# Kernel tuning notes

Measured on AMD Instinct MI355X. Metric: run time of the kernel, lower is better.

Reference implementation:

```python
import jax, jax.numpy as jnp
import numpy as np

B, N, D, F, E, K = 4, 2048, 1024, 4096, 16, 2
EPS = 1e-5  # torch LayerNorm default


def setup_inputs() -> dict:
    key = jax.random.key(0)
    ks = jax.random.split(key, 6)
    scaled = lambda k, shape, fan: jax.random.normal(k, shape, jnp.float32) / np.float32(np.sqrt(fan))
    return {
        "x": jax.random.normal(ks[0], (B, N, D), jnp.float32),
        "Wr": scaled(ks[1], (D, E), D),
        "br": jnp.zeros((E,), jnp.float32),
        "W1": scaled(ks[2], (E, D, F), D),
        "W3": scaled(ks[3], (E, D, F), D),
        "W2": scaled(ks[4], (E, F, D), F),
        "gamma": jnp.ones((E, D), jnp.float32),
        "beta": jnp.zeros((E, D), jnp.float32),
    }


def reference(x, Wr, br, W1, W3, W2, gamma, beta):
    b, n, d = x.shape
    e = Wr.shape[1]
    xf = x.reshape(-1, d)  # [T, D]

    # Router: softmax -> top-2 -> renormalize (eval mode: no noise)
    logits = xf @ Wr + br                      # [T, E]
    probs = jax.nn.softmax(logits, axis=-1)
    vals, idx = jax.lax.top_k(probs, K)        # [T, K]
    w = vals / vals.sum(axis=-1, keepdims=True)

    # Per-token per-expert combine weights [T, E] (0 for unselected experts)
    combine = jnp.zeros((xf.shape[0], e), x.dtype)
    for k in range(K):
        combine = combine + w[:, k:k + 1] * jax.nn.one_hot(idx[:, k], e, dtype=x.dtype)

    # Expert FFN (SwiGLU -> LayerNorm), weighted combine.
    # Computing each expert on all tokens and scaling by combine (0 where not
    # routed) is mathematically identical to the masked gather/scatter loop,
    # since SwiGLU+LayerNorm are per-token ops.
    out = jnp.zeros_like(xf)
    for ei in range(e):
        h = jax.nn.silu(xf @ W1[ei]) * (xf @ W3[ei])   # [T, F]
        y = h @ W2[ei]                                  # [T, D]
        mu = y.mean(axis=-1, keepdims=True)
        var = ((y - mu) ** 2).mean(axis=-1, keepdims=True)
        y = (y - mu) * jax.lax.rsqrt(var + EPS) * gamma[ei] + beta[ei]
        out = out + combine[:, ei:ei + 1] * y
    return out.reshape(b, n, d)
```

## Files before the change

### kernel.cpp

```cpp
#include <hip/hip_runtime.h>
#include <stdint.h>

#define T_TOK 8192
#define DD 1024
#define FF 4096
#define EE 16
#define BM 128
#define BN 128
#define BK 32
#define MAX_MT 144
#define MAX_SLOTS 18432

typedef __attribute__((ext_vector_type(4))) float f32x4;
typedef __attribute__((ext_vector_type(8))) short bf16x8;

__device__ __forceinline__ unsigned short f2bf(float f) {
  union { float f; unsigned u; } v; v.f = f;
  unsigned r = v.u + 0x7FFFu + ((v.u >> 16) & 1u);
  return (unsigned short)(r >> 16);
}

__device__ __forceinline__ void gload16(const void* g, void* l) {
  __builtin_amdgcn_global_load_lds(
      (const __attribute__((address_space(1))) unsigned int*)g,
      (__attribute__((address_space(3))) unsigned int*)l, 16, 0, 0);
}

__global__ void router_kernel(const float* __restrict__ x, const float* __restrict__ Wr,
                              const float* __restrict__ br,
                              int* __restrict__ counts, int* __restrict__ tok_e,
                              int* __restrict__ tok_s, float* __restrict__ tok_w,
                              int* __restrict__ elist) {
  int t = blockIdx.x * blockDim.x + threadIdx.x;
  if (t >= T_TOK) return;
  float acc[EE];
#pragma unroll
  for (int e = 0; e < EE; ++e) acc[e] = br[e];
  const f32x4* x4 = (const f32x4*)(x + (size_t)t * DD);
  for (int d4 = 0; d4 < DD / 4; ++d4) {
    f32x4 xv = x4[d4];
    const float* wr = Wr + (size_t)d4 * 4 * EE;
#pragma unroll
    for (int dd = 0; dd < 4; ++dd)
#pragma unroll
      for (int e = 0; e < EE; ++e) acc[e] += xv[dd] * wr[dd * EE + e];
  }
  int i0 = 0; float v0 = acc[0];
#pragma unroll
  for (int e = 1; e < EE; ++e) if (acc[e] > v0) { v0 = acc[e]; i0 = e; }
  int i1 = -1; float v1 = -3.4e38f;
#pragma unroll
  for (int e = 0; e < EE; ++e) if (e != i0 && acc[e] > v1) { v1 = acc[e]; i1 = e; }
  float p1 = __expf(v1 - v0);
  float w0 = 1.f / (1.f + p1);
  float w1 = p1 * w0;
  int s0 = atomicAdd(&counts[i0], 1);
  int s1 = atomicAdd(&counts[i1], 1);
  tok_e[2 * t] = i0; tok_s[2 * t] = s0; tok_w[2 * t] = w0;
  tok_e[2 * t + 1] = i1; tok_s[2 * t + 1] = s1; tok_w[2 * t + 1] = w1;
  elist[(size_t)i0 * T_TOK + s0] = t;
  elist[(size_t)i1 * T_TOK + s1] = t;
}

__global__ void scan_kernel(const int* __restrict__ counts, int* __restrict__ off,
                            int* __restrict__ mtb) {
  if (threadIdx.x == 0 && blockIdx.x == 0) {
    int o = 0, m = 0;
    for (int e = 0; e < EE; ++e) {
      off[e] = o; mtb[e] = m;
      int c = counts[e];
      int mt = (c + BM - 1) / BM;
      o += mt * BM; m += mt;
    }
    off[EE] = o; mtb[EE] = m;
  }
}

__global__ void gather_kernel(const float* __restrict__ x, const int* __restrict__ counts,
                              const int* __restrict__ off, const int* __restrict__ elist,
                              unsigned short* __restrict__ Xg) {
  int slot = blockIdx.x;
  if (slot >= off[EE]) return;
  int e = 0;
  while (e < EE - 1 && off[e + 1] <= slot) ++e;
  int s = slot - off[e];
  int tid = threadIdx.x;
  ushort4* dst = (ushort4*)(Xg + (size_t)slot * DD);
  if (s < counts[e]) {
    int t = elist[(size_t)e * T_TOK + s];
    f32x4 v = ((const f32x4*)(x + (size_t)t * DD))[tid];
    ushort4 o;
    o.x = f2bf(v[0]); o.y = f2bf(v[1]); o.z = f2bf(v[2]); o.w = f2bf(v[3]);
    dst[tid] = o;
  } else {
    ushort4 z; z.x = z.y = z.z = z.w = 0;
    dst[tid] = z;
  }
}

__global__ void transpose_conv(const float* __restrict__ src0, unsigned short* __restrict__ dst0,
                               int R, int C) {
  __shared__ float tile[64][65];
  int e = blockIdx.z;
  const float* src = src0 + (size_t)e * R * C;
  unsigned short* dst = dst0 + (size_t)e * R * C;
  int r0 = blockIdx.y * 64, c0 = blockIdx.x * 64;
  int tx = threadIdx.x & 15, ty = threadIdx.x >> 4;
#pragma unroll
  for (int i = 0; i < 4; ++i) {
    int r = i * 16 + ty;
    f32x4 v = *(const f32x4*)(src + (size_t)(r0 + r) * C + c0 + tx * 4);
    tile[r][tx * 4 + 0] = v[0]; tile[r][tx * 4 + 1] = v[1];
    tile[r][tx * 4 + 2] = v[2]; tile[r][tx * 4 + 3] = v[3];
  }
  __syncthreads();
#pragma unroll
  for (int i = 0; i < 4; ++i) {
    int c = i * 16 + ty;
    ushort4 o;
    o.x = f2bf(tile[tx * 4 + 0][c]); o.y = f2bf(tile[tx * 4 + 1][c]);
    o.z = f2bf(tile[tx * 4 + 2][c]); o.w = f2bf(tile[tx * 4 + 3][c]);
    *(ushort4*)(dst + (size_t)(c0 + c) * R + r0 + tx * 4) = o;
  }
}

__global__ __launch_bounds__(256, 2) void gemm1_kernel(
    const unsigned short* __restrict__ Xg, const unsigned short* __restrict__ W1t,
    const unsigned short* __restrict__ W3t, const int* __restrict__ off,
    const int* __restrict__ mtb, unsigned short* __restrict__ H) {
  __shared__ __align__(16) unsigned short As[BM][BK];
  __shared__ __align__(16) unsigned short B1s[BN][BK];
  __shared__ __align__(16) unsigned short B3s[BN][BK];
  int ty = blockIdx.y;
  if (ty >= mtb[EE]) return;
  int e = 0;
  while (e < EE - 1 && mtb[e + 1] <= ty) ++e;
  int m0 = off[e] + (ty - mtb[e]) * BM;
  int n0 = blockIdx.x * BN;
  const unsigned short* A = Xg + (size_t)m0 * DD;
  const unsigned short* B1 = W1t + ((size_t)e * FF + n0) * DD;
  const unsigned short* B3 = W3t + ((size_t)e * FF + n0) * DD;
  int tid = threadIdx.x, lane = tid & 63, wid = tid >> 6;
  int wm = wid >> 1, wn = wid & 1;
  f32x4 acc1[4][4] = {}; f32x4 acc3[4][4] = {};
  int fr = lane & 15, fk = (lane >> 4) * 8;
  for (int k0 = 0; k0 < DD; k0 += BK) {
#pragma unroll
    for (int r = 0; r < 2; ++r) {
      int c = r * 256 + tid;
      int row = c >> 2, ch = c & 3;
      gload16(A + (size_t)row * DD + k0 + ch * 8, (char*)As + c * 16);
      gload16(B1 + (size_t)row * DD + k0 + ch * 8, (char*)B1s + c * 16);
      gload16(B3 + (size_t)row * DD + k0 + ch * 8, (char*)B3s + c * 16);
    }
    __syncthreads();
    bf16x8 a[4], b1[4], b3[4];
#pragma unroll
    for (int mi = 0; mi < 4; ++mi) a[mi] = *(const bf16x8*)&As[wm * 64 + mi * 16 + fr][fk];
#pragma unroll
    for (int ni = 0; ni < 4; ++ni) {
      b1[ni] = *(const bf16x8*)&B1s[wn * 64 + ni * 16 + fr][fk];
      b3[ni] = *(const bf16x8*)&B3s[wn * 64 + ni * 16 + fr][fk];
    }
#pragma unroll
    for (int mi = 0; mi < 4; ++mi)
#pragma unroll
      for (int ni = 0; ni < 4; ++ni) {
        acc1[mi][ni] = __builtin_amdgcn_mfma_f32_16x16x32_bf16(a[mi], b1[ni], acc1[mi][ni], 0, 0, 0);
        acc3[mi][ni] = __builtin_amdgcn_mfma_f32_16x16x32_bf16(a[mi], b3[ni], acc3[mi][ni], 0, 0, 0);
      }
    __syncthreads();
  }
#pragma unroll
  for (int mi = 0; mi < 4; ++mi)
#pragma unroll
    for (int ni = 0; ni < 4; ++ni)
#pragma unroll
      for (int i = 0; i < 4; ++i) {
        int row = m0 + wm * 64 + mi * 16 + (lane >> 4) * 4 + i;
        int col = n0 + wn * 64 + ni * 16 + (lane & 15);
        float c1 = acc1[mi][ni][i], c3 = acc3[mi][ni][i];
        float h = c1 / (1.f + __expf(-c1)) * c3;
        H[(size_t)row * FF + col] = f2bf(h);
      }
}

__global__ __launch_bounds__(256, 2) void gemm2_kernel(
    const unsigned short* __restrict__ H, const unsigned short* __restrict__ W2t,
    const int* __restrict__ off, const int* __restrict__ mtb, float* __restrict__ Y) {
  __shared__ __align__(16) unsigned short As[BM][BK];
  __shared__ __align__(16) unsigned short Bs[BN][BK];
  int ty = blockIdx.y;
  if (ty >= mtb[EE]) return;
  int e = 0;
  while (e < EE - 1 && mtb[e + 1] <= ty) ++e;
  int m0 = off[e] + (ty - mtb[e]) * BM;
  int n0 = blockIdx.x * BN;
  const unsigned short* A = H + (size_t)m0 * FF;
  const unsigned short* B = W2t + ((size_t)e * DD + n0) * FF;
  int tid = threadIdx.x, lane = tid & 63, wid = tid >> 6;
  int wm = wid >> 1, wn = wid & 1;
  f32x4 acc[4][4] = {};
  int fr = lane & 15, fk = (lane >> 4) * 8;
  for (int k0 = 0; k0 < FF; k0 += BK) {
#pragma unroll
    for (int r = 0; r < 2; ++r) {
      int c = r * 256 + tid;
      int row = c >> 2, ch = c & 3;
      gload16(A + (size_t)row * FF + k0 + ch * 8, (char*)As + c * 16);
      gload16(B + (size_t)row * FF + k0 + ch * 8, (char*)Bs + c * 16);
    }
    __syncthreads();
    bf16x8 a[4], b[4];
#pragma unroll
    for (int mi = 0; mi < 4; ++mi) a[mi] = *(const bf16x8*)&As[wm * 64 + mi * 16 + fr][fk];
#pragma unroll
    for (int ni = 0; ni < 4; ++ni) b[ni] = *(const bf16x8*)&Bs[wn * 64 + ni * 16 + fr][fk];
#pragma unroll
    for (int mi = 0; mi < 4; ++mi)
#pragma unroll
      for (int ni = 0; ni < 4; ++ni)
        acc[mi][ni] = __builtin_amdgcn_mfma_f32_16x16x32_bf16(a[mi], b[ni], acc[mi][ni], 0, 0, 0);
    __syncthreads();
  }
#pragma unroll
  for (int mi = 0; mi < 4; ++mi)
#pragma unroll
    for (int ni = 0; ni < 4; ++ni)
#pragma unroll
      for (int i = 0; i < 4; ++i) {
        int row = m0 + wm * 64 + mi * 16 + (lane >> 4) * 4 + i;
        int col = n0 + wn * 64 + ni * 16 + (lane & 15);
        Y[(size_t)row * DD + col] = acc[mi][ni][i];
      }
}

__global__ void ln_combine_kernel(const float* __restrict__ Y, const int* __restrict__ tok_e,
                                  const int* __restrict__ tok_s, const float* __restrict__ tok_w,
                                  const int* __restrict__ off, const float* __restrict__ gamma,
                                  const float* __restrict__ beta, float* __restrict__ out) {
  int t = blockIdx.x, tid = threadIdx.x;
  __shared__ float red[8];
  f32x4 o = {0.f, 0.f, 0.f, 0.f};
  for (int k = 0; k < 2; ++k) {
    int e = tok_e[2 * t + k], s = tok_s[2 * t + k];
    float w = tok_w[2 * t + k];
    int slot = off[e] + s;
    f32x4 v = ((const f32x4*)(Y + (size_t)slot * DD))[tid];
    float sum = v[0] + v[1] + v[2] + v[3];
    float sq = v[0] * v[0] + v[1] * v[1] + v[2] * v[2] + v[3] * v[3];
    for (int d = 32; d > 0; d >>= 1) {
      sum += __shfl_down(sum, d);
      sq += __shfl_down(sq, d);
    }
    int wv = tid >> 6, lane = tid & 63;
    if (lane == 0) { red[wv * 2] = sum; red[wv * 2 + 1] = sq; }
    __syncthreads();
    float S1 = red[0] + red[2] + red[4] + red[6];
    float S2 = red[1] + red[3] + red[5] + red[7];
    __syncthreads();
    float mu = S1 * (1.f / (float)DD);
    float var = S2 * (1.f / (float)DD) - mu * mu;
    float rs = rsqrtf(var + 1e-5f);
    f32x4 g = ((const f32x4*)(gamma + (size_t)e * DD))[tid];
    f32x4 b = ((const f32x4*)(beta + (size_t)e * DD))[tid];
#pragma unroll
    for (int j = 0; j < 4; ++j) o[j] += w * ((v[j] - mu) * rs * g[j] + b[j]);
  }
  ((f32x4*)out)[(size_t)t * (DD / 4) + tid] = o;
}

extern "C" void kernel_launch(void* const* d_in, const int* in_sizes, int n_in,
                              void* d_out, int out_size, void* d_ws, size_t ws_size,
                              hipStream_t stream) {
  const float* x = (const float*)d_in[0];
  const float* Wr = (const float*)d_in[1];
  const float* br = (const float*)d_in[2];
  const float* W1 = (const float*)d_in[3];
  const float* W3 = (const float*)d_in[4];
  const float* W2 = (const float*)d_in[5];
  const float* gamma = (const float*)d_in[6];
  const float* beta = (const float*)d_in[7];
  float* out = (float*)d_out;

  char* w = (char*)d_ws;
  size_t o = 0;
  auto alloc = [&](size_t bytes) {
    void* p = w + o;
    o += (bytes + 255) & ~(size_t)255;
    return p;
  };
  int* counts = (int*)alloc(EE * 4);
  int* off = (int*)alloc((EE + 1) * 4);
  int* mtb = (int*)alloc((EE + 1) * 4);
  int* tok_e = (int*)alloc(2 * T_TOK * 4);
  int* tok_s = (int*)alloc(2 * T_TOK * 4);
  float* tok_w = (float*)alloc(2 * T_TOK * 4);
  int* elist = (int*)alloc((size_t)EE * T_TOK * 4);
  unsigned short* Xg = (unsigned short*)alloc((size_t)MAX_SLOTS * DD * 2);
  unsigned short* W1t = (unsigned short*)alloc((size_t)EE * DD * FF * 2);
  unsigned short* W3t = (unsigned short*)alloc((size_t)EE * DD * FF * 2);
  unsigned short* W2t = (unsigned short*)alloc((size_t)EE * DD * FF * 2);
  unsigned short* Hb = (unsigned short*)alloc((size_t)MAX_SLOTS * FF * 2);
  float* Y = (float*)alloc((size_t)MAX_SLOTS * DD * 4);

  hipMemsetAsync(counts, 0, EE * sizeof(int), stream);
  router_kernel<<<T_TOK / 256, 256, 0, stream>>>(x, Wr, br, counts, tok_e, tok_s, tok_w, elist);
  scan_kernel<<<1, 64, 0, stream>>>(counts, off, mtb);
  gather_kernel<<<MAX_SLOTS, 256, 0, stream>>>(x, counts, off, elist, Xg);
  transpose_conv<<<dim3(FF / 64, DD / 64, EE), 256, 0, stream>>>(W1, W1t, DD, FF);
  transpose_conv<<<dim3(FF / 64, DD / 64, EE), 256, 0, stream>>>(W3, W3t, DD, FF);
  transpose_conv<<<dim3(DD / 64, FF / 64, EE), 256, 0, stream>>>(W2, W2t, FF, DD);
  gemm1_kernel<<<dim3(FF / BN, MAX_MT), 256, 0, stream>>>(Xg, W1t, W3t, off, mtb, Hb);
  gemm2_kernel<<<dim3(DD / BN, MAX_MT), 256, 0, stream>>>(Hb, W2t, off, mtb, Y);
  ln_combine_kernel<<<T_TOK, 256, 0, stream>>>(Y, tok_e, tok_s, tok_w, off, gamma, beta, out);
}
```

Baseline: 1.085 ms.

## Rewrite gemm1 as 256x256 double-buffered tile with interleaved W1/W3 layout

```diff
diff --git a/kernel.cpp b/kernel.cpp
--- a/kernel.cpp
+++ b/kernel.cpp
@@ -5,11 +5,9 @@
 #define DD 1024
 #define FF 4096
 #define EE 16
-#define BM 128
-#define BN 128
-#define BK 32
-#define MAX_MT 144
-#define MAX_SLOTS 18432
+#define MAX_SLOTS 20480
+#define MT1 80
+#define MT2 160
 
 typedef __attribute__((ext_vector_type(4))) float f32x4;
 typedef __attribute__((ext_vector_type(8))) short bf16x8;
@@ -63,16 +61,17 @@
 }
 
 __global__ void scan_kernel(const int* __restrict__ counts, int* __restrict__ off,
-                            int* __restrict__ mtb) {
+                            int* __restrict__ mtb, int* __restrict__ mtb2) {
   if (threadIdx.x == 0 && blockIdx.x == 0) {
     int o = 0, m = 0;
     for (int e = 0; e < EE; ++e) {
       off[e] = o; mtb[e] = m;
       int c = counts[e];
-      int mt = (c + BM - 1) / BM;
-      o += mt * BM; m += mt;
+      int mt = (c + 255) / 256;
+      o += mt * 256; m += mt;
     }
     off[EE] = o; mtb[EE] = m;
+    for (int e = 0; e <= EE; ++e) mtb2[e] = off[e] >> 7;
   }
 }
 
@@ -99,11 +98,11 @@
 }
 
 __global__ void transpose_conv(const float* __restrict__ src0, unsigned short* __restrict__ dst0,
-                               int R, int C) {
+                               int R, int C, size_t dstEstride, int mode) {
   __shared__ float tile[64][65];
   int e = blockIdx.z;
   const float* src = src0 + (size_t)e * R * C;
-  unsigned short* dst = dst0 + (size_t)e * R * C;
+  unsigned short* dst = dst0 + (size_t)e * dstEstride;
   int r0 = blockIdx.y * 64, c0 = blockIdx.x * 64;
   int tx = threadIdx.x & 15, ty = threadIdx.x >> 4;
 #pragma unroll
@@ -117,92 +116,158 @@
 #pragma unroll
   for (int i = 0; i < 4; ++i) {
     int c = i * 16 + ty;
+    int cg = c0 + c;
+    int rp = (mode == 0) ? cg : ((cg >> 7) * 256 + (cg & 127) + ((mode == 2) ? 128 : 0));
     ushort4 o;
     o.x = f2bf(tile[tx * 4 + 0][c]); o.y = f2bf(tile[tx * 4 + 1][c]);
     o.z = f2bf(tile[tx * 4 + 2][c]); o.w = f2bf(tile[tx * 4 + 3][c]);
-    *(ushort4*)(dst + (size_t)(c0 + c) * R + r0 + tx * 4) = o;
-  }
-}
-
-__global__ __launch_bounds__(256, 2) void gemm1_kernel(
-    const unsigned short* __restrict__ Xg, const unsigned short* __restrict__ W1t,
-    const unsigned short* __restrict__ W3t, const int* __restrict__ off,
-    const int* __restrict__ mtb, unsigned short* __restrict__ H) {
-  __shared__ __align__(16) unsigned short As[BM][BK];
-  __shared__ __align__(16) unsigned short B1s[BN][BK];
-  __shared__ __align__(16) unsigned short B3s[BN][BK];
+    *(ushort4*)(dst + (size_t)rp * R + r0 + tx * 4) = o;
+  }
+}
+
+#define PHASE(MQ, NQ, READA)                                                        \
+  do {                                                                              \
+    if (READA) {                                                                    \
+      _Pragma("unroll") for (int mi = 0; mi < 4; ++mi) {                            \
+        int r = wr * 128 + MQ * 64 + mi * 16 + fr;                                  \
+        pa[mi][0] = *(const bf16x8*)(lds + curOff + (r << 7) + ((fkk << 1) ^ swz)); \
+        pa[mi][1] = *(const bf16x8*)(lds + curOff + (r << 7) + ((64 + (fkk << 1)) ^ swz)); \
+      }                                                                             \
+    }                                                                               \
+    _Pragma("unroll") for (int ni = 0; ni < 2; ++ni) {                              \
+      int r = wc * 64 + NQ * 32 + ni * 16 + fr;                                     \
+      pb[ni][0] = *(const bf16x8*)(lds + curOff + 32768 + (r << 7) + ((fkk << 1) ^ swz)); \
+      pb[ni][1] = *(const bf16x8*)(lds + curOff + 32768 + (r << 7) + ((64 + (fkk << 1)) ^ swz)); \
+    }                                                                               \
+    __builtin_amdgcn_s_barrier();                                                   \
+    asm volatile("s_waitcnt lgkmcnt(0)" ::: "memory");                              \
+    __builtin_amdgcn_sched_barrier(0);                                              \
+    __builtin_amdgcn_s_setprio(1);                                                  \
+    _Pragma("unroll") for (int mi = 0; mi < 4; ++mi)                                \
+      _Pragma("unroll") for (int ni = 0; ni < 2; ++ni) {                            \
+        acc[MQ * 4 + mi][NQ * 2 + ni] = __builtin_amdgcn_mfma_f32_16x16x32_bf16(    \
+            pa[mi][0], pb[ni][0], acc[MQ * 4 + mi][NQ * 2 + ni], 0, 0, 0);          \
+        acc[MQ * 4 + mi][NQ * 2 + ni] = __builtin_amdgcn_mfma_f32_16x16x32_bf16(    \
+            pa[mi][1], pb[ni][1], acc[MQ * 4 + mi][NQ * 2 + ni], 0, 0, 0);          \
+      }                                                                             \
+    __builtin_amdgcn_s_setprio(0);                                                  \
+    __builtin_amdgcn_s_barrier();                                                   \
+  } while (0)
+
+__global__ __launch_bounds__(512, 2) void gemm1_kernel(
+    const unsigned short* __restrict__ Xg, const unsigned short* __restrict__ W13t,
+    const int* __restrict__ off, const int* __restrict__ mtb,
+    unsigned short* __restrict__ H) {
+  __shared__ __align__(16) char lds[131072];
   int ty = blockIdx.y;
   if (ty >= mtb[EE]) return;
   int e = 0;
   while (e < EE - 1 && mtb[e + 1] <= ty) ++e;
-  int m0 = off[e] + (ty - mtb[e]) * BM;
-  int n0 = blockIdx.x * BN;
+  int m0 = off[e] + (ty - mtb[e]) * 256;
+  int n0s = blockIdx.x * 256;
+  int hcol0 = blockIdx.x * 128;
   const unsigned short* A = Xg + (size_t)m0 * DD;
-  const unsigned short* B1 = W1t + ((size_t)e * FF + n0) * DD;
-  const unsigned short* B3 = W3t + ((size_t)e * FF + n0) * DD;
+  const unsigned short* B = W13t + ((size_t)e * (2 * FF) + n0s) * DD;
+
   int tid = threadIdx.x, lane = tid & 63, wid = tid >> 6;
-  int wm = wid >> 1, wn = wid & 1;
-  f32x4 acc1[4][4] = {}; f32x4 acc3[4][4] = {};
-  int fr = lane & 15, fk = (lane >> 4) * 8;
-  for (int k0 = 0; k0 < DD; k0 += BK) {
-#pragma unroll
-    for (int r = 0; r < 2; ++r) {
-      int c = r * 256 + tid;
-      int row = c >> 2, ch = c & 3;
-      gload16(A + (size_t)row * DD + k0 + ch * 8, (char*)As + c * 16);
-      gload16(B1 + (size_t)row * DD + k0 + ch * 8, (char*)B1s + c * 16);
-      gload16(B3 + (size_t)row * DD + k0 + ch * 8, (char*)B3s + c * 16);
-    }
-    __syncthreads();
-    bf16x8 a[4], b1[4], b3[4];
-#pragma unroll
-    for (int mi = 0; mi < 4; ++mi) a[mi] = *(const bf16x8*)&As[wm * 64 + mi * 16 + fr][fk];
-#pragma unroll
-    for (int ni = 0; ni < 4; ++ni) {
-      b1[ni] = *(const bf16x8*)&B1s[wn * 64 + ni * 16 + fr][fk];
-      b3[ni] = *(const bf16x8*)&B3s[wn * 64 + ni * 16 + fr][fk];
-    }
-#pragma unroll
-    for (int mi = 0; mi < 4; ++mi)
-#pragma unroll
-      for (int ni = 0; ni < 4; ++ni) {
-        acc1[mi][ni] = __builtin_amdgcn_mfma_f32_16x16x32_bf16(a[mi], b1[ni], acc1[mi][ni], 0, 0, 0);
-        acc3[mi][ni] = __builtin_amdgcn_mfma_f32_16x16x32_bf16(a[mi], b3[ni], acc3[mi][ni], 0, 0, 0);
-      }
-    __syncthreads();
-  }
-#pragma unroll
-  for (int mi = 0; mi < 4; ++mi)
-#pragma unroll
-    for (int ni = 0; ni < 4; ++ni)
-#pragma unroll
-      for (int i = 0; i < 4; ++i) {
-        int row = m0 + wm * 64 + mi * 16 + (lane >> 4) * 4 + i;
-        int col = n0 + wn * 64 + ni * 16 + (lane & 15);
-        float c1 = acc1[mi][ni][i], c3 = acc3[mi][ni][i];
-        float h = c1 / (1.f + __expf(-c1)) * c3;
-        H[(size_t)row * FF + col] = f2bf(h);
-      }
+  int wr = wid >> 2, wc = wid & 3;
+  int fr = lane & 15, fkk = (lane >> 4) * 8;
+  int swz = (fr & 7) << 4;
+  int xc = ((tid & 7) ^ ((tid >> 3) & 7)) << 3;
+
+  auto stage = [&](int bufOff, int k0) {
+#pragma unroll
+    for (int j = 0; j < 4; ++j) {
+      int row = j * 64 + (tid >> 3);
+      gload16(A + (size_t)row * DD + k0 + xc, lds + bufOff + j * 8192 + tid * 16);
+      gload16(B + (size_t)row * DD + k0 + xc, lds + bufOff + 32768 + j * 8192 + tid * 16);
+    }
+  };
+
+  f32x4 acc[8][4] = {};
+  bf16x8 pa[4][2], pb[2][2];
+
+  asm volatile("s_waitcnt vmcnt(0)" ::: "memory");
+  stage(0, 0);
+  stage(65536, 64);
+  asm volatile("s_waitcnt vmcnt(8)" ::: "memory");
+  __builtin_amdgcn_s_barrier();
+
+  for (int kt = 0; kt < 16; ++kt) {
+    int curOff = (kt & 1) << 16;
+    PHASE(0, 0, 1);
+    PHASE(0, 1, 0);
+    PHASE(1, 0, 1);
+    PHASE(1, 1, 0);
+    if (kt < 14) {
+      stage(curOff, (kt + 2) * 64);
+      asm volatile("s_waitcnt vmcnt(8)" ::: "memory");
+      __builtin_amdgcn_s_barrier();
+    } else if (kt == 14) {
+      asm volatile("s_waitcnt vmcnt(0)" ::: "memory");
+      __builtin_amdgcn_s_barrier();
+    }
+  }
+
+  float* L3 = (float*)lds;
+  unsigned short* HO = (unsigned short*)(lds + 69632);
+  int frow = (lane >> 4) * 4;
+#pragma unroll 1
+  for (int h = 0; h < 2; ++h) {
+    __syncthreads();
+    if (wr == h && wc >= 2) {
+#pragma unroll
+      for (int mi = 0; mi < 8; ++mi)
+#pragma unroll
+        for (int ni = 0; ni < 4; ++ni)
+#pragma unroll
+          for (int i = 0; i < 4; ++i)
+            L3[(mi * 16 + frow + i) * 132 + (wc - 2) * 64 + ni * 16 + fr] = acc[mi][ni][i];
+    }
+    __syncthreads();
+    if (wr == h && wc < 2) {
+#pragma unroll
+      for (int mi = 0; mi < 8; ++mi)
+#pragma unroll
+        for (int ni = 0; ni < 4; ++ni)
+#pragma unroll
+          for (int i = 0; i < 4; ++i) {
+            float c1 = acc[mi][ni][i];
+            float c3 = L3[(mi * 16 + frow + i) * 132 + wc * 64 + ni * 16 + fr];
+            float hv = c1 / (1.f + __expf(-c1)) * c3;
+            HO[(mi * 16 + frow + i) * 128 + wc * 64 + ni * 16 + fr] = f2bf(hv);
+          }
+    }
+    __syncthreads();
+#pragma unroll
+    for (int s = 0; s < 4; ++s) {
+      int flat = s * 8192 + tid * 16;
+      int rr = flat >> 8, cb2 = flat & 255;
+      *(bf16x8*)(H + (size_t)(m0 + h * 128 + rr) * FF + hcol0 + (cb2 >> 1)) =
+          *(const bf16x8*)((const char*)HO + flat);
+    }
+    __syncthreads();
+  }
 }
 
 __global__ __launch_bounds__(256, 2) void gemm2_kernel(
     const unsigned short* __restrict__ H, const unsigned short* __restrict__ W2t,
-    const int* __restrict__ off, const int* __restrict__ mtb, float* __restrict__ Y) {
-  __shared__ __align__(16) unsigned short As[BM][BK];
-  __shared__ __align__(16) unsigned short Bs[BN][BK];
+    const int* __restrict__ off, const int* __restrict__ mtb2, float* __restrict__ Y) {
+  __shared__ __align__(16) unsigned short As[128][32];
+  __shared__ __align__(16) unsigned short Bs[128][32];
   int ty = blockIdx.y;
-  if (ty >= mtb[EE]) return;
+  if (ty >= mtb2[EE]) return;
   int e = 0;
-  while (e < EE - 1 && mtb[e + 1] <= ty) ++e;
-  int m0 = off[e] + (ty - mtb[e]) * BM;
-  int n0 = blockIdx.x * BN;
+  while (e < EE - 1 && mtb2[e + 1] <= ty) ++e;
+  int m0 = off[e] + (ty - mtb2[e]) * 128;
+  int n0 = blockIdx.x * 128;
   const unsigned short* A = H + (size_t)m0 * FF;
   const unsigned short* B = W2t + ((size_t)e * DD + n0) * FF;
   int tid = threadIdx.x, lane = tid & 63, wid = tid >> 6;
   int wm = wid >> 1, wn = wid & 1;
   f32x4 acc[4][4] = {};
   int fr = lane & 15, fk = (lane >> 4) * 8;
-  for (int k0 = 0; k0 < FF; k0 += BK) {
+  for (int k0 = 0; k0 < FF; k0 += 32) {
 #pragma unroll
     for (int r = 0; r < 2; ++r) {
       int c = r * 256 + tid;
@@ -293,25 +358,25 @@
   int* counts = (int*)alloc(EE * 4);
   int* off = (int*)alloc((EE + 1) * 4);
   int* mtb = (int*)alloc((EE + 1) * 4);
+  int* mtb2 = (int*)alloc((EE + 1) * 4);
   int* tok_e = (int*)alloc(2 * T_TOK * 4);
   int* tok_s = (int*)alloc(2 * T_TOK * 4);
   float* tok_w = (float*)alloc(2 * T_TOK * 4);
   int* elist = (int*)alloc((size_t)EE * T_TOK * 4);
   unsigned short* Xg = (unsigned short*)alloc((size_t)MAX_SLOTS * DD * 2);
-  unsigned short* W1t = (unsigned short*)alloc((size_t)EE * DD * FF * 2);
-  unsigned short* W3t = (unsigned short*)alloc((size_t)EE * DD * FF * 2);
+  unsigned short* W13t = (unsigned short*)alloc((size_t)EE * 2 * FF * DD * 2);
   unsigned short* W2t = (unsigned short*)alloc((size_t)EE * DD * FF * 2);
   unsigned short* Hb = (unsigned short*)alloc((size_t)MAX_SLOTS * FF * 2);
   float* Y = (float*)alloc((size_t)MAX_SLOTS * DD * 4);
 
   hipMemsetAsync(counts, 0, EE * sizeof(int), stream);
   router_kernel<<<T_TOK / 256, 256, 0, stream>>>(x, Wr, br, counts, tok_e, tok_s, tok_w, elist);
-  scan_kernel<<<1, 64, 0, stream>>>(counts, off, mtb);
+  scan_kernel<<<1, 64, 0, stream>>>(counts, off, mtb, mtb2);
   gather_kernel<<<MAX_SLOTS, 256, 0, stream>>>(x, counts, off, elist, Xg);
-  transpose_conv<<<dim3(FF / 64, DD / 64, EE), 256, 0, stream>>>(W1, W1t, DD, FF);
-  transpose_conv<<<dim3(FF / 64, DD / 64, EE), 256, 0, stream>>>(W3, W3t, DD, FF);
-  transpose_conv<<<dim3(DD / 64, FF / 64, EE), 256, 0, stream>>>(W2, W2t, FF, DD);
-  gemm1_kernel<<<dim3(FF / BN, MAX_MT), 256, 0, stream>>>(Xg, W1t, W3t, off, mtb, Hb);
-  gemm2_kernel<<<dim3(DD / BN, MAX_MT), 256, 0, stream>>>(Hb, W2t, off, mtb, Y);
+  transpose_conv<<<dim3(FF / 64, DD / 64, EE), 256, 0, stream>>>(W1, W13t, DD, FF, (size_t)2 * FF * DD, 1);
+  transpose_conv<<<dim3(FF / 64, DD / 64, EE), 256, 0, stream>>>(W3, W13t, DD, FF, (size_t)2 * FF * DD, 2);
+  transpose_conv<<<dim3(DD / 64, FF / 64, EE), 256, 0, stream>>>(W2, W2t, FF, DD, (size_t)FF * DD, 0);
+  gemm1_kernel<<<dim3(2 * FF / 256, MT1), 512, 0, stream>>>(Xg, W13t, off, mtb, Hb);
+  gemm2_kernel<<<dim3(DD / 128, MT2), 256, 0, stream>>>(Hb, W2t, off, mtb2, Y);
   ln_combine_kernel<<<T_TOK, 256, 0, stream>>>(Y, tok_e, tok_s, tok_w, off, gamma, beta, out);
 }
```

Result: slower. 1.383 ms (+27.5%).

## Widen GEMM K-tile to 64 with XOR-swizzled LDS and grouped block remap

Applied to the files above, without the earlier changes.

```diff
diff --git a/kernel.cpp b/kernel.cpp
--- a/kernel.cpp
+++ b/kernel.cpp
@@ -5,11 +5,8 @@
 #define DD 1024
 #define FF 4096
 #define EE 16
-#define BM 128
-#define BN 128
-#define BK 32
-#define MAX_MT 144
 #define MAX_SLOTS 18432
+#define MT 144
 
 typedef __attribute__((ext_vector_type(4))) float f32x4;
 typedef __attribute__((ext_vector_type(8))) short bf16x8;
@@ -69,8 +66,8 @@
     for (int e = 0; e < EE; ++e) {
       off[e] = o; mtb[e] = m;
       int c = counts[e];
-      int mt = (c + BM - 1) / BM;
-      o += mt * BM; m += mt;
+      int mt = (c + 127) / 128;
+      o += mt * 128; m += mt;
     }
     off[EE] = o; mtb[EE] = m;
   }
@@ -128,47 +125,58 @@
     const unsigned short* __restrict__ Xg, const unsigned short* __restrict__ W1t,
     const unsigned short* __restrict__ W3t, const int* __restrict__ off,
     const int* __restrict__ mtb, unsigned short* __restrict__ H) {
-  __shared__ __align__(16) unsigned short As[BM][BK];
-  __shared__ __align__(16) unsigned short B1s[BN][BK];
-  __shared__ __align__(16) unsigned short B3s[BN][BK];
-  int ty = blockIdx.y;
-  if (ty >= mtb[EE]) return;
+  __shared__ __align__(16) char lds[49152];
+  int p = blockIdx.x + (blockIdx.y << 5);
+  int bx = (p & 255) >> 3;
+  int by = ((p >> 8) << 3) + (p & 7);
+  if (by >= mtb[EE]) return;
   int e = 0;
-  while (e < EE - 1 && mtb[e + 1] <= ty) ++e;
-  int m0 = off[e] + (ty - mtb[e]) * BM;
-  int n0 = blockIdx.x * BN;
+  while (e < EE - 1 && mtb[e + 1] <= by) ++e;
+  int m0 = off[e] + (by - mtb[e]) * 128;
+  int n0 = bx * 128;
   const unsigned short* A = Xg + (size_t)m0 * DD;
   const unsigned short* B1 = W1t + ((size_t)e * FF + n0) * DD;
   const unsigned short* B3 = W3t + ((size_t)e * FF + n0) * DD;
   int tid = threadIdx.x, lane = tid & 63, wid = tid >> 6;
   int wm = wid >> 1, wn = wid & 1;
-  f32x4 acc1[4][4] = {}; f32x4 acc3[4][4] = {};
-  int fr = lane & 15, fk = (lane >> 4) * 8;
-  for (int k0 = 0; k0 < DD; k0 += BK) {
-#pragma unroll
-    for (int r = 0; r < 2; ++r) {
-      int c = r * 256 + tid;
-      int row = c >> 2, ch = c & 3;
-      gload16(A + (size_t)row * DD + k0 + ch * 8, (char*)As + c * 16);
-      gload16(B1 + (size_t)row * DD + k0 + ch * 8, (char*)B1s + c * 16);
-      gload16(B3 + (size_t)row * DD + k0 + ch * 8, (char*)B3s + c * 16);
-    }
-    __syncthreads();
-    bf16x8 a[4], b1[4], b3[4];
-#pragma unroll
-    for (int mi = 0; mi < 4; ++mi) a[mi] = *(const bf16x8*)&As[wm * 64 + mi * 16 + fr][fk];
-#pragma unroll
-    for (int ni = 0; ni < 4; ++ni) {
-      b1[ni] = *(const bf16x8*)&B1s[wn * 64 + ni * 16 + fr][fk];
-      b3[ni] = *(const bf16x8*)&B3s[wn * 64 + ni * 16 + fr][fk];
-    }
-#pragma unroll
-    for (int mi = 0; mi < 4; ++mi)
+  int fr = lane & 15, fk4 = lane >> 4;
+  int swz = fr & 7;
+  int ce8 = (((tid & 7) ^ ((tid >> 3) & 7)) << 3);
+  const unsigned short* AgT = A + (size_t)(tid >> 3) * DD + ce8;
+  const unsigned short* B1T = B1 + (size_t)(tid >> 3) * DD + ce8;
+  const unsigned short* B3T = B3 + (size_t)(tid >> 3) * DD + ce8;
+  char* ldsW = lds + tid * 16;
+
+  f32x4 acc1[4][4] = {}, acc3[4][4] = {};
+
+  for (int k0 = 0; k0 < DD; k0 += 64) {
+#pragma unroll
+    for (int j = 0; j < 4; ++j) {
+      gload16(AgT + (size_t)j * 32 * DD + k0, ldsW + j * 4096);
+      gload16(B1T + (size_t)j * 32 * DD + k0, ldsW + 16384 + j * 4096);
+      gload16(B3T + (size_t)j * 32 * DD + k0, ldsW + 32768 + j * 4096);
+    }
+    __syncthreads();
+#pragma unroll
+    for (int kk = 0; kk < 2; ++kk) {
+      int pc = ((kk * 4 + fk4) ^ swz) << 4;
+      bf16x8 a[4], b1[4], b3[4];
+#pragma unroll
+      for (int mi = 0; mi < 4; ++mi)
+        a[mi] = *(const bf16x8*)(lds + (wm * 64 + mi * 16 + fr) * 128 + pc);
 #pragma unroll
       for (int ni = 0; ni < 4; ++ni) {
-        acc1[mi][ni] = __builtin_amdgcn_mfma_f32_16x16x32_bf16(a[mi], b1[ni], acc1[mi][ni], 0, 0, 0);
-        acc3[mi][ni] = __builtin_amdgcn_mfma_f32_16x16x32_bf16(a[mi], b3[ni], acc3[mi][ni], 0, 0, 0);
+        b1[ni] = *(const bf16x8*)(lds + 16384 + (wn * 64 + ni * 16 + fr) * 128 + pc);
+        b3[ni] = *(const bf16x8*)(lds + 32768 + (wn * 64 + ni * 16 + fr) * 128 + pc);
       }
+#pragma unroll
+      for (int mi = 0; mi < 4; ++mi)
+#pragma unroll
+        for (int ni = 0; ni < 4; ++ni) {
+          acc1[mi][ni] = __builtin_amdgcn_mfma_f32_16x16x32_bf16(a[mi], b1[ni], acc1[mi][ni], 0, 0, 0);
+          acc3[mi][ni] = __builtin_amdgcn_mfma_f32_16x16x32_bf16(a[mi], b3[ni], acc3[mi][ni], 0, 0, 0);
+        }
+    }
     __syncthreads();
   }
 #pragma unroll
@@ -188,39 +196,51 @@
 __global__ __launch_bounds__(256, 2) void gemm2_kernel(
     const unsigned short* __restrict__ H, const unsigned short* __restrict__ W2t,
     const int* __restrict__ off, const int* __restrict__ mtb, float* __restrict__ Y) {
-  __shared__ __align__(16) unsigned short As[BM][BK];
-  __shared__ __align__(16) unsigned short Bs[BN][BK];
-  int ty = blockIdx.y;
-  if (ty >= mtb[EE]) return;
+  __shared__ __align__(16) char lds[32768];
+  int p = blockIdx.x + (blockIdx.y << 3);
+  int bx = (p & 63) >> 3;
+  int by = ((p >> 6) << 3) + (p & 7);
+  if (by >= mtb[EE]) return;
   int e = 0;
-  while (e < EE - 1 && mtb[e + 1] <= ty) ++e;
-  int m0 = off[e] + (ty - mtb[e]) * BM;
-  int n0 = blockIdx.x * BN;
+  while (e < EE - 1 && mtb[e + 1] <= by) ++e;
+  int m0 = off[e] + (by - mtb[e]) * 128;
+  int n0 = bx * 128;
   const unsigned short* A = H + (size_t)m0 * FF;
   const unsigned short* B = W2t + ((size_t)e * DD + n0) * FF;
   int tid = threadIdx.x, lane = tid & 63, wid = tid >> 6;
   int wm = wid >> 1, wn = wid & 1;
+  int fr = lane & 15, fk4 = lane >> 4;
+  int swz = fr & 7;
+  int ce8 = (((tid & 7) ^ ((tid >> 3) & 7)) << 3);
+  const unsigned short* AgT = A + (size_t)(tid >> 3) * FF + ce8;
+  const unsigned short* BgT = B + (size_t)(tid >> 3) * FF + ce8;
+  char* ldsW = lds + tid * 16;
+
   f32x4 acc[4][4] = {};
-  int fr = lane & 15, fk = (lane >> 4) * 8;
-  for (int k0 = 0; k0 < FF; k0 += BK) {
-#pragma unroll
-    for (int r = 0; r < 2; ++r) {
-      int c = r * 256 + tid;
-      int row = c >> 2, ch = c & 3;
-      gload16(A + (size_t)row * FF + k0 + ch * 8, (char*)As + c * 16);
-      gload16(B + (size_t)row * FF + k0 + ch * 8, (char*)Bs + c * 16);
-    }
-    __syncthreads();
-    bf16x8 a[4], b[4];
-#pragma unroll
-    for (int mi = 0; mi < 4; ++mi) a[mi] = *(const bf16x8*)&As[wm * 64 + mi * 16 + fr][fk];
-#pragma unroll
-    for (int ni = 0; ni < 4; ++ni) b[ni] = *(const bf16x8*)&Bs[wn * 64 + ni * 16 + fr][fk];
-#pragma unroll
-    for (int mi = 0; mi < 4; ++mi)
+
+  for (int k0 = 0; k0 < FF; k0 += 64) {
+#pragma unroll
+    for (int j = 0; j < 4; ++j) {
+      gload16(AgT + (size_t)j * 32 * FF + k0, ldsW + j * 4096);
+      gload16(BgT + (size_t)j * 32 * FF + k0, ldsW + 16384 + j * 4096);
+    }
+    __syncthreads();
+#pragma unroll
+    for (int kk = 0; kk < 2; ++kk) {
+      int pc = ((kk * 4 + fk4) ^ swz) << 4;
+      bf16x8 a[4], b[4];
+#pragma unroll
+      for (int mi = 0; mi < 4; ++mi)
+        a[mi] = *(const bf16x8*)(lds + (wm * 64 + mi * 16 + fr) * 128 + pc);
 #pragma unroll
       for (int ni = 0; ni < 4; ++ni)
-        acc[mi][ni] = __builtin_amdgcn_mfma_f32_16x16x32_bf16(a[mi], b[ni], acc[mi][ni], 0, 0, 0);
+        b[ni] = *(const bf16x8*)(lds + 16384 + (wn * 64 + ni * 16 + fr) * 128 + pc);
+#pragma unroll
+      for (int mi = 0; mi < 4; ++mi)
+#pragma unroll
+        for (int ni = 0; ni < 4; ++ni)
+          acc[mi][ni] = __builtin_amdgcn_mfma_f32_16x16x32_bf16(a[mi], b[ni], acc[mi][ni], 0, 0, 0);
+    }
     __syncthreads();
   }
 #pragma unroll
@@ -311,7 +331,7 @@
   transpose_conv<<<dim3(FF / 64, DD / 64, EE), 256, 0, stream>>>(W1, W1t, DD, FF);
   transpose_conv<<<dim3(FF / 64, DD / 64, EE), 256, 0, stream>>>(W3, W3t, DD, FF);
   transpose_conv<<<dim3(DD / 64, FF / 64, EE), 256, 0, stream>>>(W2, W2t, FF, DD);
-  gemm1_kernel<<<dim3(FF / BN, MAX_MT), 256, 0, stream>>>(Xg, W1t, W3t, off, mtb, Hb);
-  gemm2_kernel<<<dim3(DD / BN, MAX_MT), 256, 0, stream>>>(Hb, W2t, off, mtb, Y);
+  gemm1_kernel<<<dim3(FF / 128, MT), 256, 0, stream>>>(Xg, W1t, W3t, off, mtb, Hb);
+  gemm2_kernel<<<dim3(DD / 128, MT), 256, 0, stream>>>(Hb, W2t, off, mtb, Y);
   ln_combine_kernel<<<T_TOK, 256, 0, stream>>>(Y, tok_e, tok_s, tok_w, off, gamma, beta, out);
 }
```

New measurement: 1.004 ms. 1.08x faster.
